# Kernel tuning notes

Hardware: AMD Instinct MI355X
Metric: run time of the kernel (lower is better)

Reference implementation:

```python
import jax, jax.numpy as jnp
import numpy as np
from jax import lax

SHIFT = 32  # shift_range from init
EPS_NORM = 1e-12
EPS_MASK = 1e-6


def _l2_normalize_flat(x):
    # F.normalize(x.reshape(B,-1)): per-sample L2 normalize with eps 1e-12
    B = x.shape[0]
    flat = x.reshape(B, -1)
    n = jnp.linalg.norm(flat, axis=1, keepdims=True)
    return (flat / jnp.maximum(n, EPS_NORM)).reshape(x.shape)


def setup_inputs() -> dict:
    key = jax.random.key(0)
    k1, k2 = jax.random.split(key)
    grd_feature = jax.random.normal(k1, (8, 32, 32, 32), dtype=jnp.float32)
    sat_feature = jax.random.normal(k2, (8, 32, 128, 128), dtype=jnp.float32)
    return {"grd_feature": grd_feature, "sat_feature": sat_feature, "test_method": 1}


def reference(grd_feature, sat_feature, test_method):
    # test_method == 1 path (default); test_method in {0,1} only differ in divisor
    M, C, H_s, W_s = sat_feature.shape
    N, _, H, W = grd_feature.shape
    kH = min(H, H_s - 2 * SHIFT)
    kW = min(W, W_s - 2 * SHIFT)

    # center-crop ground template to (kH, kW) and L2-normalize per sample
    gh0, gw0 = H // 2 - kH // 2, W // 2 - kW // 2
    grd = grd_feature[:, :, gh0:gh0 + 2 * (kH // 2), gw0:gw0 + 2 * (kW // 2)]
    N_, _, H_k, W_k = grd.shape
    grd = _l2_normalize_flat(grd)

    # center-crop satellite to search region and L2-normalize per sample
    sh0 = H_s // 2 - SHIFT - kH // 2
    sw0 = W_s // 2 - SHIFT - kW // 2
    sat = sat_feature[:, :, sh0:sh0 + 2 * (SHIFT + kH // 2), sw0:sw0 + 2 * (SHIFT + kW // 2)]
    _, _, H_i, W_i = sat.shape
    sat = _l2_normalize_flat(sat)

    # all-pairs cross-correlation: corr[m, n, y, x] (torch grouped-conv on repeated sat
    # is equivalent to a plain VALID conv of sat with all N ground filters)
    corr = lax.conv_general_dilated(
        sat, grd, window_strides=(1, 1), padding='VALID',
        dimension_numbers=('NCHW', 'OIHW', 'NCHW'))  # [M, N, Ho, Wo]
    Ho, Wo = corr.shape[2], corr.shape[3]

    # sliding-window sum of |sat|^2 (avg_pool with divisor_override=1, summed over C)
    s2 = jnp.sum(sat * sat, axis=1)  # [M, H_i, W_i]
    partical = lax.reduce_window(s2, jnp.float32(0), lax.add,
                                 (1, H_k, W_k), (1, 1, 1), 'VALID')  # [M, Ho, Wo]
    if test_method == 0:
        denom = jnp.sqrt(partical)
    else:
        denom = partical
    corr = corr / jnp.maximum(denom[:, None], EPS_NORM)

    similarity_matrix = jnp.max(corr, axis=(2, 3))  # [M, N]

    # diagonal pairs (m == n): peak localization
    diag = jnp.diagonal(corr, axis1=0, axis2=1)        # [Ho, Wo, M]
    diag = jnp.transpose(diag, (2, 0, 1)).reshape(M, -1)
    max_index = jnp.argmax(diag, axis=-1)
    pos_h = max_index // Wo
    pos_w = max_index % Wo

    grd_mask = (jnp.abs(jnp.sum(grd, axis=1)) > EPS_MASK).astype(jnp.float32)  # [N, H_k, W_k]

    def place(ph, pw, gm):
        z = jnp.zeros((1, H_i, W_i), dtype=jnp.float32)
        return lax.dynamic_update_slice(z, gm[None], (0, ph, pw))

    mask = jax.vmap(place)(pos_h, pos_w, grd_mask)  # [M, 1, H_i, W_i]
    return similarity_matrix, mask
```

## Files before the change

kernel.cpp:

```cpp
#include <hip/hip_runtime.h>
#include <stdint.h>

typedef unsigned short u16;
typedef unsigned int u32;
typedef __bf16 bf16x8 __attribute__((ext_vector_type(8)));
typedef float floatx4 __attribute__((ext_vector_type(4)));

#define DEVI static __device__ __forceinline__

DEVI u16 f2bf(float f) {
  uint32_t u = __builtin_bit_cast(uint32_t, f);
  u += 0x7FFFu + ((u >> 16) & 1u);
  return (u16)(u >> 16);
}
DEVI float bf2f(u16 b) { return __builtin_bit_cast(float, (uint32_t)b << 16); }

static constexpr size_t OFF_CORRP = 0;
static constexpr size_t OFF_SATT  = OFF_CORRP + (size_t)4*270400*4;
static constexpr size_t OFF_GRDP  = OFF_SATT + (size_t)8*4*96*96*8*2;
static constexpr size_t OFF_S2    = OFF_GRDP + (size_t)4*1024*16*8*2;
static constexpr size_t OFF_PART  = OFF_S2   + (size_t)73728*4;
static constexpr size_t OFF_NRMP  = OFF_PART + (size_t)33800*4;
static constexpr size_t OFF_GNRM  = OFF_NRMP + 768*4;
static constexpr size_t OFF_MASK  = OFF_GNRM + 32;
static constexpr size_t OFF_VDIAG = OFF_MASK + (size_t)8192*4;
static constexpr size_t OFF_PMAX  = OFF_VDIAG + (size_t)33800*4;

__global__ __launch_bounds__(256) void k_prep(
    const float* __restrict__ grd, const float* __restrict__ sat,
    u16* __restrict__ sTh, u16* __restrict__ gP,
    float* __restrict__ s2, float* __restrict__ nrmp,
    float* __restrict__ gnrm, float* __restrict__ gmask) {
  __shared__ float L[32*100];
  __shared__ float red[256];
  const int t = threadIdx.x;
  if (blockIdx.x < 768) {
    const int m = blockIdx.x / 96, y = blockIdx.x - (blockIdx.x / 96) * 96;
    #pragma unroll
    for (int k = 0; k < 3; ++k) {
      const int idx = k*256 + t;
      const int c = idx / 24, xq = idx - c*24;
      const float4 v = *(const float4*)(sat + (((size_t)m*32 + c)*128 + (16+y))*128 + 16 + xq*4);
      *(float4*)(&L[c*100 + xq*4]) = v;
    }
    __syncthreads();
    float ss = 0.f;
    if (t < 96) {
      #pragma unroll
      for (int c = 0; c < 32; ++c) { const float v = L[c*100 + t]; ss += v*v; }
      s2[(size_t)m*9216 + y*96 + t] = ss;
    }
    red[t] = ss; __syncthreads();
    for (int s = 128; s > 0; s >>= 1) { if (t < s) red[t] += red[t+s]; __syncthreads(); }
    if (t == 0) nrmp[m*96 + y] = red[0];
    for (int idx = t; idx < 384; idx += 256) {
      const int cb = idx / 96, x = idx - cb*96;
      union { u16 us[8]; uint4 v4; } P;
      #pragma unroll
      for (int e = 0; e < 8; ++e) P.us[e] = f2bf(L[(cb*8+e)*100 + x]);
      *(uint4*)(&sTh[(((size_t)m*4+cb)*9216 + (size_t)y*96 + x)*8]) = P.v4;
    }
  } else {
    const int n = blockIdx.x - 768;
    float nn = 0.f, scs[4];
    #pragma unroll
    for (int it = 0; it < 4; ++it) {
      const int pidx = it*256 + t;
      float vals[32]; float sc = 0.f;
      #pragma unroll
      for (int c = 0; c < 32; ++c) {
        const float v = grd[((size_t)n*32 + c)*1024 + pidx];
        vals[c] = v; sc += v; nn += v*v;
      }
      scs[it] = sc;
      #pragma unroll
      for (int cb = 0; cb < 4; ++cb) {
        union { u16 us[8]; uint4 v4; } ph, pl;
        #pragma unroll
        for (int e = 0; e < 8; ++e) {
          const float v = vals[cb*8+e];
          const u16 h = f2bf(v); ph.us[e] = h; pl.us[e] = f2bf(v - bf2f(h));
        }
        const size_t o = ((size_t)cb*1024 + pidx)*128;
        *(uint4*)(&gP[o + (size_t)n*8])     = ph.v4;
        *(uint4*)(&gP[o + (size_t)(n+8)*8]) = pl.v4;
      }
    }
    red[t] = nn; __syncthreads();
    for (int s = 128; s > 0; s >>= 1) { if (t < s) red[t] += red[t+s]; __syncthreads(); }
    const float gn = fmaxf(sqrtf(red[0]), 1e-12f);
    if (t == 0) gnrm[n] = red[0];
    const float thr = 1e-6f * gn;
    #pragma unroll
    for (int it = 0; it < 4; ++it)
      gmask[n*1024 + it*256 + t] = (fabsf(scs[it]) > thr) ? 1.f : 0.f;
  }
}

__global__ __launch_bounds__(256, 4) void k_conv(
    const u16* __restrict__ satT, const u16* __restrict__ gP,
    const float* __restrict__ s2, float* __restrict__ corr_p,
    float* __restrict__ part)
{
  __shared__ __align__(16) u16 patch[36*48*8];

  int bi = blockIdx.x;
  const int tid = threadIdx.x;

  if (bi >= 2080) {
    float* S  = (float*)patch;
    float* HS = S + 40*96;
    const int pb = bi - 2080;
    const int pm = pb / 9, ysl = (pb - pm*9)*8;
    const int nrows = (65 - ysl) < 8 ? (65 - ysl) : 8;
    const int scnt  = (96 - ysl) < 40 ? (96 - ysl) : 40;
    for (int idx = tid; idx < scnt*96; idx += 256)
      S[idx] = s2[(size_t)pm*9216 + (size_t)ysl*96 + idx];
    __syncthreads();
    const int hrows = nrows + 31;
    for (int idx = tid; idx < hrows*65; idx += 256) {
      const int r = idx / 65, xo = idx - r*65;
      const float* p = &S[r*96 + xo];
      float s = 0.f;
      #pragma unroll
      for (int j = 0; j < 32; ++j) s += p[j];
      HS[idx] = s;
    }
    __syncthreads();
    for (int idx = tid; idx < nrows*65; idx += 256) {
      const int r = idx / 65, xo = idx - r*65;
      float s = 0.f;
      #pragma unroll
      for (int i = 0; i < 32; ++i) s += HS[(r+i)*65 + xo];
      part[(size_t)pm*4225 + (size_t)(ysl+r)*65 + xo] = s;
    }
    return;
  }

  const int cb = bi & 3; bi >>= 2;
  const int xt = bi % 5; bi /= 5;
  const int yt = bi % 13;
  const int m  = bi / 13;
  const int y0 = yt*5, x0 = xt*16;
  const int wave = tid >> 6, lane = tid & 63;

  {
    const size_t rowbase = ((size_t)(m*4 + cb) * 96 + y0) * 96;
    for (int k = tid; k < 36*48; k += 256) {
      const int rho = k / 48;
      const int px  = k - rho*48;
      int X = x0 + px; if (X > 95) X = 95;
      *(uint4*)(&patch[(size_t)k*8]) = *(const uint4*)(&satT[(rowbase + (size_t)rho*96 + X)*8]);
    }
  }
  __syncthreads();

  const int pr = lane & 15;
  const int q  = lane >> 4;

  floatx4 acc[5];
  #pragma unroll
  for (int r = 0; r < 5; ++r) acc[r] = (floatx4){0.f, 0.f, 0.f, 0.f};

  #pragma unroll
  for (int jbi = 0; jbi < 2; ++jbi) {
    const int jb = wave*2 + jbi;
    const int apx = pr + jb*4 + q;
    const u16* bp = gP + ((size_t)cb*1024 + (size_t)(jb*4+q))*128 + (size_t)pr*8;

    uint4 Br[8];
    #pragma unroll
    for (int ii = 0; ii < 8; ++ii) Br[ii] = *(const uint4*)(bp + (size_t)ii*4096);
    uint4 Ah[8];
    #pragma unroll
    for (int s = 0; s < 6; ++s) Ah[s] = *(const uint4*)(&patch[((size_t)s*48 + apx)*8]);

    #pragma unroll
    for (int i = 0; i < 32; ++i) {
      if (i < 30)
        Ah[(i+6)&7] = *(const uint4*)(&patch[((size_t)(i+6)*48 + apx)*8]);
      const bf16x8 bf = __builtin_bit_cast(bf16x8, Br[i&7]);
      if (i < 24)
        Br[(i+8)&7] = *(const uint4*)(bp + (size_t)(i+8)*4096);
      #pragma unroll
      for (int r = 0; r < 5; ++r)
        acc[r] = __builtin_amdgcn_mfma_f32_16x16x32_bf16(
            __builtin_bit_cast(bf16x8, Ah[(i+r)&7]), bf, acc[r], 0, 0, 0);
    }
  }

  float vals[20];
  #pragma unroll
  for (int r = 0; r < 5; ++r)
    #pragma unroll
    for (int e = 0; e < 4; ++e)
      vals[r*4+e] = acc[r][e] + __shfl_xor(acc[r][e], 8);

  __syncthreads();
  float* red = (float*)patch;
  #pragma unroll
  for (int u = 0; u < 20; ++u) red[((size_t)wave*64 + lane)*21 + u] = vals[u];
  __syncthreads();
  if (wave == 0 && pr < 8) {
    #pragma unroll
    for (int r = 0; r < 5; ++r) {
      #pragma unroll
      for (int e = 0; e < 4; ++e) {
        const int x = x0 + q*4 + e;
        if (x < 65) {
          float s = 0.f;
          #pragma unroll
          for (int w = 0; w < 4; ++w) s += red[((size_t)w*64 + lane)*21 + r*4 + e];
          corr_p[(size_t)cb*270400 + ((size_t)(m*8+pr)*65 + (y0+r))*65 + x] = s;
        }
      }
    }
  }
}

__global__ __launch_bounds__(256) void k_vmax(
    const float* __restrict__ corr_p, const float* __restrict__ part,
    const float* __restrict__ nrmp, const float* __restrict__ gnrm,
    const int* __restrict__ tm, float* __restrict__ vdiag,
    float* __restrict__ pmax)
{
  __shared__ float red[256];
  const int bi = blockIdx.x;
  const int m = bi / 40, n = (bi / 5) & 7, yc = bi % 5;
  const int t = threadIdx.x;
  red[t] = (t < 96) ? nrmp[m*96 + t] : 0.f;
  __syncthreads();
  for (int s = 128; s > 0; s >>= 1) { if (t < s) red[t] += red[t+s]; __syncthreads(); }
  const float srn = 1.f / fmaxf(sqrtf(red[0]), 1e-12f);
  const float grn = 1.f / fmaxf(sqrtf(gnrm[n]), 1e-12f);
  const float cscale = grn * srn, pscale = srn * srn;
  const int method = tm[0];
  const float* cp = corr_p + (size_t)(m*8+n)*4225;
  const float* pp = part + (size_t)m*4225;
  const int i0 = yc*845, i1 = i0 + 845;
  const bool diag = (m == n);
  float bestv = -3.4e38f;
  for (int idx = i0 + t; idx < i1; idx += 256) {
    const float c = cp[idx] + cp[idx+270400] + cp[idx+540800] + cp[idx+811200];
    const float pt = pp[idx] * pscale;
    float denom = (method == 0) ? sqrtf(pt) : pt;
    denom = fmaxf(denom, 1e-12f);
    const float v = c * cscale / denom;
    if (diag) vdiag[(size_t)m*4225 + idx] = v;
    bestv = fmaxf(bestv, v);
  }
  __syncthreads();
  red[t] = bestv; __syncthreads();
  for (int s = 128; s > 0; s >>= 1) { if (t < s) red[t] = fmaxf(red[t], red[t+s]); __syncthreads(); }
  if (t == 0) pmax[bi] = red[0];
}

__global__ __launch_bounds__(256) void k_out(
    const float* __restrict__ vdiag, const float* __restrict__ pmax,
    const float* __restrict__ grd, const float* __restrict__ sat,
    const float* __restrict__ part, const float* __restrict__ nrmp,
    const float* __restrict__ gnrm, const int* __restrict__ tm,
    const float* __restrict__ gmask, float* __restrict__ out)
{
  const int t = threadIdx.x;
  if (blockIdx.x == 8) {
    if (t < 64) {
      float v = pmax[t*5];
      #pragma unroll
      for (int k = 1; k < 5; ++k) v = fmaxf(v, pmax[t*5 + k]);
      out[t] = v;
    }
    return;
  }
  const int n = blockIdx.x;
  __shared__ float red[256];
  __shared__ int cands[64];
  __shared__ int ccnt;
  __shared__ float sbest; __shared__ int sbix;

  red[t] = (t < 96) ? nrmp[n*96 + t] : 0.f;
  __syncthreads();
  for (int s = 128; s > 0; s >>= 1) { if (t < s) red[t] += red[t+s]; __syncthreads(); }
  const float srn = 1.f / fmaxf(sqrtf(red[0]), 1e-12f);
  const float grn = 1.f / fmaxf(sqrtf(gnrm[n]), 1e-12f);
  const float cscale = grn * srn, pscale = srn * srn;
  const int method = tm[0];

  float vm = pmax[n*45];
  #pragma unroll
  for (int k = 1; k < 5; ++k) vm = fmaxf(vm, pmax[n*45 + k]);
  if (t == 0) { ccnt = 0; sbest = -3.4e38f; sbix = 0x7FFFFFFF; }
  __syncthreads();
  const float thr = vm - 3e-3f;
  const float* vd = vdiag + (size_t)n*4225;
  for (int idx = t; idx < 4225; idx += 256)
    if (vd[idx] >= thr) { const int s = atomicAdd(&ccnt, 1); if (s < 64) cands[s] = idx; }
  __syncthreads();
  int nc = ccnt; if (nc > 64) nc = 64; if (nc < 1) nc = 1;

  const int c = t >> 3, s8 = t & 7;
  for (int ci = 0; ci < nc; ++ci) {
    const int idx = cands[ci];
    const int y = idx / 65, x = idx - y*65;
    float a = 0.f;
    #pragma unroll
    for (int ii = 0; ii < 4; ++ii) {
      const int i = s8 + ii*8;
      const float* gr = grd + ((size_t)n*32 + c)*1024 + i*32;
      const float* sr = sat + (((size_t)n*32 + c)*128 + (16 + y + i))*128 + (16 + x);
      #pragma unroll
      for (int j = 0; j < 32; ++j) a += gr[j] * sr[j];
    }
    red[t] = a; __syncthreads();
    for (int st = 128; st > 0; st >>= 1) { if (t < st) red[t] += red[t+st]; __syncthreads(); }
    if (t == 0) {
      const float pt = part[(size_t)n*4225 + idx] * pscale;
      float denom = (method == 0) ? sqrtf(pt) : pt;
      denom = fmaxf(denom, 1e-12f);
      const float v = red[0] * cscale / denom;
      if (v > sbest || (v == sbest && idx < sbix)) { sbest = v; sbix = idx; }
    }
    __syncthreads();
  }
  const int bix = sbix;
  const int ph = bix / 65, pw = bix - (bix/65)*65;
  for (int p = t; p < 1024; p += 256)
    out[64 + (size_t)n*9216 + (size_t)(ph + (p>>5))*96 + (pw + (p&31))] = gmask[n*1024 + p];
}

extern "C" void kernel_launch(void* const* d_in, const int* in_sizes, int n_in,
                              void* d_out, int out_size, void* d_ws, size_t ws_size,
                              hipStream_t stream) {
  const float* grd = (const float*)d_in[0];
  const float* sat = (const float*)d_in[1];
  const int*   tm  = (const int*)d_in[2];
  float* out = (float*)d_out;
  char* ws = (char*)d_ws;

  float* corrp = (float*)(ws + OFF_CORRP);
  u16*   sTh   = (u16*)(ws + OFF_SATT);
  u16*   gP    = (u16*)(ws + OFF_GRDP);
  float* s2    = (float*)(ws + OFF_S2);
  float* part  = (float*)(ws + OFF_PART);
  float* nrmp  = (float*)(ws + OFF_NRMP);
  float* gnrm  = (float*)(ws + OFF_GNRM);
  float* gmask = (float*)(ws + OFF_MASK);
  float* vdiag = (float*)(ws + OFF_VDIAG);
  float* pmax  = (float*)(ws + OFF_PMAX);

  hipMemsetAsync(d_out, 0, (size_t)out_size * sizeof(float), stream);

  k_prep<<<776,  256, 0, stream>>>(grd, sat, sTh, gP, s2, nrmp, gnrm, gmask);
  k_conv<<<2152, 256, 0, stream>>>(sTh, gP, s2, corrp, part);
  k_vmax<<<320,  256, 0, stream>>>(corrp, part, nrmp, gnrm, tm, vdiag, pmax);
  k_out <<<9,    256, 0, stream>>>(vdiag, pmax, grd, sat, part, nrmp, gnrm, tm, gmask, out);
}
```

Baseline: 154.5 us.

## Fuse post-processing into one kernel and add dedicated last-column conv blocks

The final two kernels are merged into a single post kernel. It uses a last-block-arrives atomic counter to reduce the per-pair maxima and pick diagonal candidates, so the vdiag buffer and a kernel launch go away. The conv grid is reorganized: the main tiles now cover x 0..63 exactly with no clamping, and a new set of blocks computes the single x=64 column with a 13-row MFMA layout, removing the 5th partially wasted x-tile. The output memset is dropped because the mask kernel now writes the full plane, including zeros. The change adds atomic complexity and a serial tail in the last-arriving blocks.

```diff
diff --git a/kernel.cpp b/kernel.cpp
--- a/kernel.cpp
+++ b/kernel.cpp
@@ -3,6 +3,7 @@
 
 typedef unsigned short u16;
 typedef unsigned int u32;
+typedef unsigned long long u64;
 typedef __bf16 bf16x8 __attribute__((ext_vector_type(8)));
 typedef float floatx4 __attribute__((ext_vector_type(4)));
 
@@ -14,6 +15,15 @@
   return (u16)(u >> 16);
 }
 DEVI float bf2f(u16 b) { return __builtin_bit_cast(float, (uint32_t)b << 16); }
+
+DEVI u32 encf(float f) {
+  u32 u = __builtin_bit_cast(u32, f);
+  return (u >> 31) ? ~u : (u | 0x80000000u);
+}
+DEVI float decf(u32 e) {
+  u32 u = (e >> 31) ? (e & 0x7FFFFFFFu) : ~e;
+  return __builtin_bit_cast(float, u);
+}
 
 static constexpr size_t OFF_CORRP = 0;
 static constexpr size_t OFF_SATT  = OFF_CORRP + (size_t)4*270400*4;
@@ -23,14 +33,16 @@
 static constexpr size_t OFF_NRMP  = OFF_PART + (size_t)33800*4;
 static constexpr size_t OFF_GNRM  = OFF_NRMP + 768*4;
 static constexpr size_t OFF_MASK  = OFF_GNRM + 32;
-static constexpr size_t OFF_VDIAG = OFF_MASK + (size_t)8192*4;
-static constexpr size_t OFF_PMAX  = OFF_VDIAG + (size_t)33800*4;
+static constexpr size_t OFF_PMAX  = OFF_MASK + (size_t)8192*4;
+static constexpr size_t OFF_CNT   = OFF_PMAX + 320*4;
+static constexpr size_t OFF_CAND  = OFF_CNT  + 512;
 
 __global__ __launch_bounds__(256) void k_prep(
     const float* __restrict__ grd, const float* __restrict__ sat,
     u16* __restrict__ sTh, u16* __restrict__ gP,
     float* __restrict__ s2, float* __restrict__ nrmp,
-    float* __restrict__ gnrm, float* __restrict__ gmask) {
+    float* __restrict__ gnrm, float* __restrict__ gmask,
+    u32* __restrict__ cnts) {
   __shared__ float L[32*100];
   __shared__ float red[256];
   const int t = threadIdx.x;
@@ -60,6 +72,8 @@
       for (int e = 0; e < 8; ++e) P.us[e] = f2bf(L[(cb*8+e)*100 + x]);
       *(uint4*)(&sTh[(((size_t)m*4+cb)*9216 + (size_t)y*96 + x)*8]) = P.v4;
     }
+  } else if (blockIdx.x == 776) {
+    if (t < 72) cnts[t] = 0u;
   } else {
     const int n = blockIdx.x - 768;
     float nn = 0.f, scs[4];
@@ -104,13 +118,13 @@
 {
   __shared__ __align__(16) u16 patch[36*48*8];
 
-  int bi = blockIdx.x;
+  const int bi = blockIdx.x;
   const int tid = threadIdx.x;
 
-  if (bi >= 2080) {
+  if (bi >= 1824) {
     float* S  = (float*)patch;
     float* HS = S + 40*96;
-    const int pb = bi - 2080;
+    const int pb = bi - 1824;
     const int pm = pb / 9, ysl = (pb - pm*9)*8;
     const int nrows = (65 - ysl) < 8 ? (65 - ysl) : 8;
     const int scnt  = (96 - ysl) < 40 ? (96 - ysl) : 40;
@@ -137,26 +151,87 @@
     return;
   }
 
-  const int cb = bi & 3; bi >>= 2;
-  const int xt = bi % 5; bi /= 5;
-  const int yt = bi % 13;
-  const int m  = bi / 13;
+  const int wave = tid >> 6, lane = tid & 63;
+  const int pr = lane & 15, q = lane >> 4;
+
+  if (bi >= 1664) {
+    const int e = bi - 1664;
+    const int cb = e & 3;
+    const int yt = (e >> 2) % 5;
+    const int m  = e / 20;
+    const int ybase = yt * 13;
+    const size_t rowbase = ((size_t)(m*4 + cb) * 96 + ybase) * 96;
+    for (int k = tid; k < 44*32; k += 256) {
+      const int rho = k >> 5, px = k & 31;
+      *(uint4*)(&patch[(size_t)k*8]) =
+          *(const uint4*)(&satT[(rowbase + (size_t)rho*96 + 64 + px)*8]);
+    }
+    __syncthreads();
+    const int prc = pr < 13 ? pr : 12;
+    floatx4 acc = (floatx4){0.f, 0.f, 0.f, 0.f};
+    #pragma unroll
+    for (int jbi = 0; jbi < 2; ++jbi) {
+      const int jb = wave*2 + jbi;
+      const int px_e = jb*4 + q;
+      const u16* bp = gP + ((size_t)cb*1024 + (size_t)(jb*4+q))*128 + (size_t)pr*8;
+      uint4 Br[8];
+      #pragma unroll
+      for (int ii = 0; ii < 8; ++ii) Br[ii] = *(const uint4*)(bp + (size_t)ii*4096);
+      uint4 Ah[8];
+      #pragma unroll
+      for (int s = 0; s < 6; ++s)
+        Ah[s] = *(const uint4*)(&patch[((size_t)(prc + s)*32 + px_e)*8]);
+      #pragma unroll
+      for (int i = 0; i < 32; ++i) {
+        if (i < 26)
+          Ah[(i+6)&7] = *(const uint4*)(&patch[((size_t)(prc + i + 6)*32 + px_e)*8]);
+        const bf16x8 bf = __builtin_bit_cast(bf16x8, Br[i&7]);
+        if (i < 24)
+          Br[(i+8)&7] = *(const uint4*)(bp + (size_t)(i+8)*4096);
+        acc = __builtin_amdgcn_mfma_f32_16x16x32_bf16(
+            __builtin_bit_cast(bf16x8, Ah[i&7]), bf, acc, 0, 0, 0);
+      }
+    }
+    float v4[4];
+    #pragma unroll
+    for (int k = 0; k < 4; ++k) v4[k] = acc[k] + __shfl_xor(acc[k], 8);
+    __syncthreads();
+    float* red = (float*)patch;
+    #pragma unroll
+    for (int k = 0; k < 4; ++k) red[((size_t)wave*64 + lane)*5 + k] = v4[k];
+    __syncthreads();
+    if (wave == 0 && pr < 8) {
+      #pragma unroll
+      for (int k = 0; k < 4; ++k) {
+        const int yoff = q*4 + k;
+        if (yoff < 13) {
+          float s = 0.f;
+          #pragma unroll
+          for (int w = 0; w < 4; ++w) s += red[((size_t)w*64 + lane)*5 + k];
+          corr_p[(size_t)cb*270400 + ((size_t)(m*8+pr)*65 + (ybase+yoff))*65 + 64] = s;
+        }
+      }
+    }
+    return;
+  }
+
+  int b = bi;
+  const int cb = b & 3; b >>= 2;
+  const int xt = b % 4; b /= 4;
+  const int yt = b % 13;
+  const int m  = b / 13;
   const int y0 = yt*5, x0 = xt*16;
-  const int wave = tid >> 6, lane = tid & 63;
 
   {
     const size_t rowbase = ((size_t)(m*4 + cb) * 96 + y0) * 96;
     for (int k = tid; k < 36*48; k += 256) {
       const int rho = k / 48;
       const int px  = k - rho*48;
-      int X = x0 + px; if (X > 95) X = 95;
-      *(uint4*)(&patch[(size_t)k*8]) = *(const uint4*)(&satT[(rowbase + (size_t)rho*96 + X)*8]);
-    }
-  }
-  __syncthreads();
-
-  const int pr = lane & 15;
-  const int q  = lane >> 4;
+      *(uint4*)(&patch[(size_t)k*8]) =
+          *(const uint4*)(&satT[(rowbase + (size_t)rho*96 + x0 + px)*8]);
+    }
+  }
+  __syncthreads();
 
   floatx4 acc[5];
   #pragma unroll
@@ -193,8 +268,8 @@
   #pragma unroll
   for (int r = 0; r < 5; ++r)
     #pragma unroll
-    for (int e = 0; e < 4; ++e)
-      vals[r*4+e] = acc[r][e] + __shfl_xor(acc[r][e], 8);
+    for (int k = 0; k < 4; ++k)
+      vals[r*4+k] = acc[r][k] + __shfl_xor(acc[r][k], 8);
 
   __syncthreads();
   float* red = (float*)patch;
@@ -205,29 +280,37 @@
     #pragma unroll
     for (int r = 0; r < 5; ++r) {
       #pragma unroll
-      for (int e = 0; e < 4; ++e) {
-        const int x = x0 + q*4 + e;
-        if (x < 65) {
-          float s = 0.f;
-          #pragma unroll
-          for (int w = 0; w < 4; ++w) s += red[((size_t)w*64 + lane)*21 + r*4 + e];
-          corr_p[(size_t)cb*270400 + ((size_t)(m*8+pr)*65 + (y0+r))*65 + x] = s;
-        }
-      }
-    }
-  }
-}
-
-__global__ __launch_bounds__(256) void k_vmax(
+      for (int k = 0; k < 4; ++k) {
+        const int x = x0 + q*4 + k;
+        float s = 0.f;
+        #pragma unroll
+        for (int w = 0; w < 4; ++w) s += red[((size_t)w*64 + lane)*21 + r*4 + k];
+        corr_p[(size_t)cb*270400 + ((size_t)(m*8+pr)*65 + (y0+r))*65 + x] = s;
+      }
+    }
+  }
+}
+
+__global__ __launch_bounds__(256) void k_post(
     const float* __restrict__ corr_p, const float* __restrict__ part,
     const float* __restrict__ nrmp, const float* __restrict__ gnrm,
-    const int* __restrict__ tm, float* __restrict__ vdiag,
-    float* __restrict__ pmax)
+    const int* __restrict__ tm, const float* __restrict__ grd,
+    const float* __restrict__ sat, const float* __restrict__ gmask,
+    u32* __restrict__ pmaxE, u32* __restrict__ grpcnt,
+    u32* __restrict__ candcnt, u64* __restrict__ cand,
+    float* __restrict__ out)
 {
   __shared__ float red[256];
+  __shared__ float s_bcast;
+  __shared__ int s_last;
+  __shared__ int fidx[128];
+  __shared__ u32 fcnt;
+
   const int bi = blockIdx.x;
-  const int m = bi / 40, n = (bi / 5) & 7, yc = bi % 5;
+  const int m = bi / 40, n = (bi / 5) & 7, yc = bi % 5, g = m*8 + n;
   const int t = threadIdx.x;
+  const bool diag = (m == n);
+
   red[t] = (t < 96) ? nrmp[m*96 + t] : 0.f;
   __syncthreads();
   for (int s = 128; s > 0; s >>= 1) { if (t < s) red[t] += red[t+s]; __syncthreads(); }
@@ -235,72 +318,81 @@
   const float grn = 1.f / fmaxf(sqrtf(gnrm[n]), 1e-12f);
   const float cscale = grn * srn, pscale = srn * srn;
   const int method = tm[0];
-  const float* cp = corr_p + (size_t)(m*8+n)*4225;
+
+  const float* cp = corr_p + (size_t)g*4225;
   const float* pp = part + (size_t)m*4225;
   const int i0 = yc*845, i1 = i0 + 845;
-  const bool diag = (m == n);
+  float vv[4];
   float bestv = -3.4e38f;
-  for (int idx = i0 + t; idx < i1; idx += 256) {
-    const float c = cp[idx] + cp[idx+270400] + cp[idx+540800] + cp[idx+811200];
-    const float pt = pp[idx] * pscale;
-    float denom = (method == 0) ? sqrtf(pt) : pt;
-    denom = fmaxf(denom, 1e-12f);
-    const float v = c * cscale / denom;
-    if (diag) vdiag[(size_t)m*4225 + idx] = v;
+  #pragma unroll
+  for (int k = 0; k < 4; ++k) {
+    const int idx = i0 + k*256 + t;
+    float v = -3.4e38f;
+    if (idx < i1) {
+      const float c = cp[idx] + cp[idx+270400] + cp[idx+540800] + cp[idx+811200];
+      const float pt = pp[idx] * pscale;
+      float denom = (method == 0) ? sqrtf(pt) : pt;
+      denom = fmaxf(denom, 1e-12f);
+      v = c * cscale / denom;
+    }
+    vv[k] = v;
     bestv = fmaxf(bestv, v);
   }
   __syncthreads();
   red[t] = bestv; __syncthreads();
   for (int s = 128; s > 0; s >>= 1) { if (t < s) red[t] = fmaxf(red[t], red[t+s]); __syncthreads(); }
-  if (t == 0) pmax[bi] = red[0];
-}
-
-__global__ __launch_bounds__(256) void k_out(
-    const float* __restrict__ vdiag, const float* __restrict__ pmax,
-    const float* __restrict__ grd, const float* __restrict__ sat,
-    const float* __restrict__ part, const float* __restrict__ nrmp,
-    const float* __restrict__ gnrm, const int* __restrict__ tm,
-    const float* __restrict__ gmask, float* __restrict__ out)
-{
-  const int t = threadIdx.x;
-  if (blockIdx.x == 8) {
-    if (t < 64) {
-      float v = pmax[t*5];
-      #pragma unroll
-      for (int k = 1; k < 5; ++k) v = fmaxf(v, pmax[t*5 + k]);
-      out[t] = v;
-    }
-    return;
-  }
-  const int n = blockIdx.x;
-  __shared__ float red[256];
-  __shared__ int cands[64];
-  __shared__ int ccnt;
+  if (t == 0) { s_bcast = red[0]; atomicExch(&pmaxE[bi], encf(red[0])); }
+  __syncthreads();
+  if (diag) {
+    const float lthr = s_bcast - 3e-3f;
+    #pragma unroll
+    for (int k = 0; k < 4; ++k) {
+      const int idx = i0 + k*256 + t;
+      if (idx < i1 && vv[k] >= lthr) {
+        const u32 s = atomicAdd(&candcnt[n], 1u);
+        if (s < 128)
+          atomicExch(&cand[n*128 + s],
+                     ((u64)__builtin_bit_cast(u32, vv[k]) << 32) | (u32)idx);
+      }
+    }
+  }
+  __syncthreads();
+  if (t == 0) s_last = (atomicAdd(&grpcnt[g], 1u) == 4u) ? 1 : 0;
+  __syncthreads();
+  if (!s_last) return;
+
+  if (t == 0) {
+    float gm = -3.4e38f;
+    #pragma unroll
+    for (int k = 0; k < 5; ++k) gm = fmaxf(gm, decf(atomicOr(&pmaxE[g*5 + k], 0u)));
+    out[g] = gm;
+    s_bcast = gm;
+  }
+  __syncthreads();
+  if (!diag) return;
+
+  const float gmax = s_bcast;
+  const float thr = gmax - 3e-3f;
+  if (t == 0) fcnt = 0u;
+  __syncthreads();
+  u32 nc = atomicAdd(&candcnt[n], 0u); if (nc > 128) nc = 128;
+  if (t < (int)nc) {
+    const u64 pk = atomicAdd(&cand[n*128 + t], 0ULL);
+    const float vf = __builtin_bit_cast(float, (u32)(pk >> 32));
+    const int idx = (int)(u32)pk;
+    if (vf >= thr) { const u32 s = atomicAdd(&fcnt, 1u); fidx[s] = idx; }
+  }
+  __syncthreads();
+  if (t == 0 && fcnt == 0u) { fidx[0] = 0; fcnt = 1u; }
+  __syncthreads();
+  const int nf = (int)fcnt;
+
   __shared__ float sbest; __shared__ int sbix;
-
-  red[t] = (t < 96) ? nrmp[n*96 + t] : 0.f;
-  __syncthreads();
-  for (int s = 128; s > 0; s >>= 1) { if (t < s) red[t] += red[t+s]; __syncthreads(); }
-  const float srn = 1.f / fmaxf(sqrtf(red[0]), 1e-12f);
-  const float grn = 1.f / fmaxf(sqrtf(gnrm[n]), 1e-12f);
-  const float cscale = grn * srn, pscale = srn * srn;
-  const int method = tm[0];
-
-  float vm = pmax[n*45];
-  #pragma unroll
-  for (int k = 1; k < 5; ++k) vm = fmaxf(vm, pmax[n*45 + k]);
-  if (t == 0) { ccnt = 0; sbest = -3.4e38f; sbix = 0x7FFFFFFF; }
-  __syncthreads();
-  const float thr = vm - 3e-3f;
-  const float* vd = vdiag + (size_t)n*4225;
-  for (int idx = t; idx < 4225; idx += 256)
-    if (vd[idx] >= thr) { const int s = atomicAdd(&ccnt, 1); if (s < 64) cands[s] = idx; }
-  __syncthreads();
-  int nc = ccnt; if (nc > 64) nc = 64; if (nc < 1) nc = 1;
-
+  if (t == 0) { sbest = -3.4e38f; sbix = 0x7FFFFFFF; }
+  __syncthreads();
   const int c = t >> 3, s8 = t & 7;
-  for (int ci = 0; ci < nc; ++ci) {
-    const int idx = cands[ci];
+  for (int ci = 0; ci < nf; ++ci) {
+    const int idx = fidx[ci];
     const int y = idx / 65, x = idx - y*65;
     float a = 0.f;
     #pragma unroll
@@ -324,8 +416,13 @@
   }
   const int bix = sbix;
   const int ph = bix / 65, pw = bix - (bix/65)*65;
-  for (int p = t; p < 1024; p += 256)
-    out[64 + (size_t)n*9216 + (size_t)(ph + (p>>5))*96 + (pw + (p&31))] = gmask[n*1024 + p];
+  for (int p = t; p < 9216; p += 256) {
+    const int yy = p / 96, xx = p - yy*96;
+    float val = 0.f;
+    if (yy >= ph && yy < ph+32 && xx >= pw && xx < pw+32)
+      val = gmask[n*1024 + (yy-ph)*32 + (xx-pw)];
+    out[64 + (size_t)n*9216 + p] = val;
+  }
 }
 
 extern "C" void kernel_launch(void* const* d_in, const int* in_sizes, int n_in,
@@ -345,13 +442,12 @@
   float* nrmp  = (float*)(ws + OFF_NRMP);
   float* gnrm  = (float*)(ws + OFF_GNRM);
   float* gmask = (float*)(ws + OFF_MASK);
-  float* vdiag = (float*)(ws + OFF_VDIAG);
-  float* pmax  = (float*)(ws + OFF_PMAX);
-
-  hipMemsetAsync(d_out, 0, (size_t)out_size * sizeof(float), stream);
-
-  k_prep<<<776,  256, 0, stream>>>(grd, sat, sTh, gP, s2, nrmp, gnrm, gmask);
-  k_conv<<<2152, 256, 0, stream>>>(sTh, gP, s2, corrp, part);
-  k_vmax<<<320,  256, 0, stream>>>(corrp, part, nrmp, gnrm, tm, vdiag, pmax);
-  k_out <<<9,    256, 0, stream>>>(vdiag, pmax, grd, sat, part, nrmp, gnrm, tm, gmask, out);
-}
+  u32*   pmaxE = (u32*)(ws + OFF_PMAX);
+  u32*   cnts  = (u32*)(ws + OFF_CNT);
+  u64*   cand  = (u64*)(ws + OFF_CAND);
+
+  k_prep<<<777,  256, 0, stream>>>(grd, sat, sTh, gP, s2, nrmp, gnrm, gmask, cnts);
+  k_conv<<<1896, 256, 0, stream>>>(sTh, gP, s2, corrp, part);
+  k_post<<<320,  256, 0, stream>>>(corrp, part, nrmp, gnrm, tm, grd, sat, gmask,
+                                   pmaxE, cnts, cnts + 64, cand, out);
+}
```

Measured after the change: 148.9 us. 3.7% less time.
